# Performance work log

Hardware: AMD Instinct MI355X
Metric: run time of the kernel (lower is better)

Reference implementation:

```python
import jax, jax.numpy as jnp
import numpy as np

# ---- static configuration (from SSN.configure) ----
B, H, W = 2, 512, 512
N_SV = 1024
Kh = int(np.floor(np.sqrt(float(N_SV) * H / W)))  # 32
Kw = int(np.floor(np.sqrt(float(N_SV) * W / H)))  # 32
K = Kh * Kw                                       # 1024
P_SCALE = 0.4
LAB_SCALE = 0.26
SOFTSCALE = -1.0
NUM_STEPS = 5
YX_SCALE = max(Kh / (P_SCALE * H), Kw / (P_SCALE * W))
INVALID_DIST = 1e10


def setup_inputs() -> dict:
    key = jax.random.key(0)
    img_lab = jax.random.normal(key, (B, 3, H, W), dtype=jnp.float32)
    # regular-grid initial superpixel index, as SSN initializes it
    ys = (jnp.arange(H, dtype=jnp.int32) * Kh) // H   # (H,) in [0,Kh)
    xs = (jnp.arange(W, dtype=jnp.int32) * Kw) // W   # (W,) in [0,Kw)
    init = ys[:, None] * Kw + xs[None, :]             # (H,W) in [0,K)
    init_spIndx = jnp.broadcast_to(init, (B, H, W))
    return {"img_lab": img_lab, "init_spIndx": init_spIndx}


def _pfeat_yxlab(img_lab):
    # (B,5,H,W): scaled Y, X positions + scaled LAB color
    Y = jnp.broadcast_to(jnp.arange(H, dtype=img_lab.dtype)[None, None, :, None], (B, 1, H, W))
    X = jnp.broadcast_to(jnp.arange(W, dtype=img_lab.dtype)[None, None, None, :], (B, 1, H, W))
    return jnp.concatenate([YX_SCALE * Y, YX_SCALE * X, LAB_SCALE * img_lab], axis=1)


def _neighbor_indices(init_spIndx):
    # 3x3 superpixel-grid neighborhood of each pixel's init superpixel
    ki = init_spIndx // Kw  # (B,H,W)
    kj = init_spIndx % Kw
    offs = jnp.array([(di, dj) for di in (-1, 0, 1) for dj in (-1, 0, 1)], dtype=jnp.int32)  # (9,2)
    ni = ki[:, None] + offs[:, 0][None, :, None, None]  # (B,9,H,W)
    nj = kj[:, None] + offs[:, 1][None, :, None, None]
    valid = (ni >= 0) & (ni < Kh) & (nj >= 0) & (nj < Kw)
    idx = jnp.clip(ni, 0, Kh - 1) * Kw + jnp.clip(nj, 0, Kw - 1)  # (B,9,H,W) in [0,K)
    return idx, valid


def _seg_sum(vals, idx):
    # vals (B, C, N), idx (B, N) -> (B, C, K)
    return jax.vmap(lambda v, i: jax.ops.segment_sum(v.T, i, num_segments=K).T)(vals, idx)


def _sp_feat_gather(pFeat, init_spIndx):
    # spFeatGather2d: per-superpixel mean of pixel features -> (B,C,K)
    C = pFeat.shape[1]
    pf = pFeat.reshape(B, C, H * W)
    ix = init_spIndx.reshape(B, H * W)
    fsum = _seg_sum(pf, ix)
    cnt = jax.vmap(lambda i: jax.ops.segment_sum(jnp.ones((H * W,), jnp.float32), i, num_segments=K))(ix)
    return fsum / jnp.maximum(cnt, 1.0)[:, None, :]


def _psp_assoc(pFeat, spFeat, idx, valid):
    # softmax over 9 local superpixels of scaled squared distance
    nbr = jax.vmap(lambda sf, ix: sf[:, ix])(spFeat, idx)          # (B,C,9,H,W)
    dist = jnp.sum((pFeat[:, :, None] - nbr) ** 2, axis=1)          # (B,9,H,W)
    dist = jnp.where(valid, dist, INVALID_DIST)
    return jax.nn.softmax(SOFTSCALE * dist, axis=1)


def _sp_feat_update(pFeat, assoc, idx, valid):
    # spFeatUpdate2d: association-weighted scatter-mean into superpixels
    C = pFeat.shape[1]
    w = jnp.where(valid, assoc, 0.0)                                # (B,9,H,W)
    contrib = (pFeat[:, :, None] * w[:, None]).reshape(B, C, 9 * H * W)
    flat_i = idx.reshape(B, 9 * H * W)
    fsum = _seg_sum(contrib, flat_i)                                # (B,C,K)
    wsum = jax.vmap(lambda wv, i: jax.ops.segment_sum(wv, i, num_segments=K))(w.reshape(B, -1), flat_i)
    return fsum / jnp.maximum(wsum, 1e-10)[:, None, :]


def reference(img_lab, init_spIndx):
    pFeat = _pfeat_yxlab(img_lab)                      # (B,5,H,W)
    idx, valid = _neighbor_indices(init_spIndx)        # (B,9,H,W)
    spFeat = _sp_feat_gather(pFeat, init_spIndx)       # (B,5,K)
    for _ in range(1, NUM_STEPS):
        assoc = _psp_assoc(pFeat, spFeat, idx, valid)
        spFeat = _sp_feat_update(pFeat, assoc, idx, valid)
    psp_assoc = _psp_assoc(pFeat, spFeat, idx, valid)  # (B,9,H,W)
    rel = jnp.argmax(psp_assoc, axis=1)                # (B,H,W)
    final_spIndx = jnp.take_along_axis(idx, rel[:, None], axis=1)[:, 0]  # (B,H,W)
    return pFeat, spFeat, psp_assoc, final_spIndx
```

## Files before the change

### kernel.cpp

```cpp
#include <hip/hip_runtime.h>

namespace {
constexpr int B = 2, H = 512, W = 512;
constexpr int KH = 32, KW = 32, K = 1024;
constexpr int HW = H * W;
constexpr float YX_SCALE = 0.15625f;
constexpr float LAB_SCALE = 0.26f;
}

template <int CTRL>
__device__ __forceinline__ float dpp_add(float v) {
  int r = __builtin_amdgcn_update_dpp(0, __float_as_int(v), CTRL, 0xF, 0xF, true);
  return v + __int_as_float(r);
}
__device__ __forceinline__ float wave_sum64(float v) {
  v = dpp_add<0xB1>(v);
  v = dpp_add<0x4E>(v);
  v = dpp_add<0x141>(v);
  v = dpp_add<0x140>(v);
  v = dpp_add<0x142>(v);
  v = dpp_add<0x143>(v);
  return v;
}

__device__ __forceinline__ float fast_rcp(float x) { return __builtin_amdgcn_rcpf(x); }

__device__ __forceinline__ float gather54(const float* __restrict__ pin,
                                          int b, int ki, int kj, int lane) {
  float g = 0.0f;
  const int n = lane / 6, comp = lane % 6;
  const int nki = ki + n / 3 - 1, nkj = kj + n % 3 - 1;
  if ((unsigned)nki < (unsigned)KH && (unsigned)nkj < (unsigned)KW) {
#pragma unroll
    for (int j = 0; j < 9; ++j) {
      const int ci = nki - (j / 3 - 1), cj = nkj - (j % 3 - 1);
      if ((unsigned)ci < (unsigned)KH && (unsigned)cj < (unsigned)KW)
        g += pin[(size_t)((b << 10) + (ci << 5) + cj) * 54 + j * 6 + comp];
    }
  }
  return g;
}

__global__ __launch_bounds__(256) void ssn_init(const float* __restrict__ lab,
                                                float* __restrict__ outPFeat,
                                                float* __restrict__ partial) {
  const int cell = blockIdx.x;
  const int b = cell >> 10;
  const int k = cell & (K - 1);
  const int ki = k >> 5, kj = k & 31;
  const int t = threadIdx.x;
  const int y = (ki << 4) + (t >> 4);
  const int x = (kj << 4) + (t & 15);
  const int pix = y * W + x;
  const float* labB = lab + (size_t)b * 3 * HW;

  float f[5];
  f[0] = YX_SCALE * (float)y;
  f[1] = YX_SCALE * (float)x;
  f[2] = LAB_SCALE * labB[pix];
  f[3] = LAB_SCALE * labB[HW + pix];
  f[4] = LAB_SCALE * labB[2 * HW + pix];

  float* po = outPFeat + (size_t)b * 5 * HW + pix;
#pragma unroll
  for (int c = 0; c < 5; ++c) po[(size_t)c * HW] = f[c];

  if (t < 54 && (t < 24 || t >= 30)) partial[(size_t)cell * 54 + t] = 0.0f;

  float s[5];
#pragma unroll
  for (int c = 0; c < 5; ++c) s[c] = wave_sum64(f[c]);
  __shared__ float red[4][5];
  if ((t & 63) == 63) {
#pragma unroll
    for (int c = 0; c < 5; ++c) red[t >> 6][c] = s[c];
  }
  __syncthreads();
  if (t < 5)
    partial[(size_t)cell * 54 + 25 + t] = red[0][t] + red[1][t] + red[2][t] + red[3][t];
  if (t == 5) partial[(size_t)cell * 54 + 24] = 256.0f;
}

__global__ __launch_bounds__(256) void ssn_update2(const float* __restrict__ lab,
                                                   const float* __restrict__ pin,
                                                   float* __restrict__ pout) {
  __shared__ float sfg[2][54];
  __shared__ float comb[2][2][54];
  const int lane = threadIdx.x & 63;
  const int wid = threadIdx.x >> 6;
  const int cidx = wid >> 1, sub = wid & 1;
  const int cell = blockIdx.x * 2 + cidx;
  const int b = cell >> 10;
  const int k = cell & (K - 1);
  const int ki = k >> 5, kj = k & 31;

  if (wid < 2 && lane < 54) {
    const int gcell = blockIdx.x * 2 + wid;
    const int gk = gcell & (K - 1);
    sfg[wid][lane] = gather54(pin, gcell >> 10, gk >> 5, gk & 31, lane);
  }
  __syncthreads();

  float sf[9][5];
  bool valid[9];
#pragma unroll
  for (int n = 0; n < 9; ++n) {
    const int ni = ki + n / 3 - 1, nj = kj + n % 3 - 1;
    valid[n] = ((unsigned)ni < (unsigned)KH) && ((unsigned)nj < (unsigned)KW);
    const float inv = fast_rcp(fmaxf(sfg[cidx][n * 6], 1e-10f));
#pragma unroll
    for (int c = 0; c < 5; ++c) sf[n][c] = sfg[cidx][n * 6 + 1 + c] * inv;
  }

  float acc[54];
#pragma unroll
  for (int i = 0; i < 54; ++i) acc[i] = 0.0f;

  const float* labB = lab + (size_t)b * 3 * HW;
#pragma unroll
  for (int pxi = 0; pxi < 2; ++pxi) {
    const int t = lane + sub * 64 + pxi * 128;
    const int y = (ki << 4) + (t >> 4);
    const int x = (kj << 4) + (t & 15);
    const int pix = y * W + x;
    float f[5];
    f[0] = YX_SCALE * (float)y;
    f[1] = YX_SCALE * (float)x;
    f[2] = LAB_SCALE * labB[pix];
    f[3] = LAB_SCALE * labB[HW + pix];
    f[4] = LAB_SCALE * labB[2 * HW + pix];

    float d[9];
#pragma unroll
    for (int j = 0; j < 9; ++j) {
      float t0 = f[0] - sf[j][0];
      float dd = t0 * t0;
#pragma unroll
      for (int c = 1; c < 5; ++c) {
        const float tc = f[c] - sf[j][c];
        dd = fmaf(tc, tc, dd);
      }
      d[j] = dd;
    }
    float m = 1e30f;
#pragma unroll
    for (int j = 0; j < 9; ++j)
      if (valid[j]) m = fminf(m, d[j]);
    float e[9], sum = 0.0f;
#pragma unroll
    for (int j = 0; j < 9; ++j) {
      e[j] = valid[j] ? __expf(m - d[j]) : 0.0f;
      sum += e[j];
    }
    const float inv = fast_rcp(sum);
#pragma unroll
    for (int j = 0; j < 9; ++j) {
      const float w = e[j] * inv;
      acc[j * 6 + 0] += w;
#pragma unroll
      for (int c = 0; c < 5; ++c)
        acc[j * 6 + 1 + c] = fmaf(w, f[c], acc[j * 6 + 1 + c]);
    }
  }

#pragma unroll
  for (int i = 0; i < 54; ++i) acc[i] = wave_sum64(acc[i]);
  if (lane == 63) {
#pragma unroll
    for (int i = 0; i < 54; ++i) comb[sub][cidx][i] = acc[i];
  }
  __syncthreads();
  if (wid < 2 && lane < 54) {
    const int scell = blockIdx.x * 2 + wid;
    pout[(size_t)scell * 54 + lane] = comb[0][wid][lane] + comb[1][wid][lane];
  }
}

__global__ __launch_bounds__(256) void ssn_final2(const float* __restrict__ lab,
                                                  const float* __restrict__ pin,
                                                  float* __restrict__ outSpFeat,
                                                  float* __restrict__ outAssoc,
                                                  float* __restrict__ outIdx) {
  __shared__ float sfg[54];
  const int tid = threadIdx.x;
  const int cell = blockIdx.x;
  const int b = cell >> 10;
  const int k = cell & (K - 1);
  const int ki = k >> 5, kj = k & 31;

  if (tid < 54) sfg[tid] = gather54(pin, b, ki, kj, tid);
  __syncthreads();

  if (tid < 5) {
    const float inv4 = 1.0f / fmaxf(sfg[24], 1e-10f);
    outSpFeat[((size_t)b * 5 + tid) * K + k] = sfg[25 + tid] * inv4;
  }

  float sf[9][5];
  bool valid[9];
#pragma unroll
  for (int n = 0; n < 9; ++n) {
    const int ni = ki + n / 3 - 1, nj = kj + n % 3 - 1;
    valid[n] = ((unsigned)ni < (unsigned)KH) && ((unsigned)nj < (unsigned)KW);
    const float inv = 1.0f / fmaxf(sfg[n * 6], 1e-10f);
#pragma unroll
    for (int c = 0; c < 5; ++c) sf[n][c] = sfg[n * 6 + 1 + c] * inv;
  }

  const int y = (ki << 4) + (tid >> 4);
  const int x = (kj << 4) + (tid & 15);
  const int pix = y * W + x;
  const float* labB = lab + (size_t)b * 3 * HW;
  float f[5];
  f[0] = YX_SCALE * (float)y;
  f[1] = YX_SCALE * (float)x;
  f[2] = LAB_SCALE * labB[pix];
  f[3] = LAB_SCALE * labB[HW + pix];
  f[4] = LAB_SCALE * labB[2 * HW + pix];

  float d[9];
#pragma unroll
  for (int j = 0; j < 9; ++j) {
    float t0 = f[0] - sf[j][0];
    float dd = t0 * t0;
#pragma unroll
    for (int c = 1; c < 5; ++c) {
      const float tc = f[c] - sf[j][c];
      dd = fmaf(tc, tc, dd);
    }
    d[j] = dd;
  }
  float m = 1e30f;
#pragma unroll
  for (int j = 0; j < 9; ++j)
    if (valid[j]) m = fminf(m, d[j]);
  float e[9], sum = 0.0f;
#pragma unroll
  for (int j = 0; j < 9; ++j) {
    e[j] = valid[j] ? __expf(m - d[j]) : 0.0f;
    sum += e[j];
  }
  const float inv = 1.0f / sum;

  float* oa = outAssoc + (size_t)b * 9 * HW + pix;
#pragma unroll
  for (int j = 0; j < 9; ++j) oa[(size_t)j * HW] = e[j] * inv;

  int bestj = 4;
  float bestd = 1e30f;
#pragma unroll
  for (int j = 0; j < 9; ++j)
    if (valid[j] && d[j] < bestd) { bestd = d[j]; bestj = j; }
  const int bi = ki + bestj / 3 - 1;
  const int bj = kj + bestj % 3 - 1;
  outIdx[(size_t)b * HW + pix] = (float)(bi * KW + bj);
}

extern "C" void kernel_launch(void* const* d_in, const int* in_sizes, int n_in,
                              void* d_out, int out_size, void* d_ws, size_t ws_size,
                              hipStream_t stream) {
  const float* lab = (const float*)d_in[0];

  float* out = (float*)d_out;
  float* outPFeat = out;
  float* outSpFeat = outPFeat + 2621440;
  float* outAssoc = outSpFeat + 10240;
  float* outIdx = outAssoc + 4718592;

  float* pA = (float*)d_ws;
  float* pB = pA + (size_t)B * K * 54;

  ssn_init<<<B * K, 256, 0, stream>>>(lab, outPFeat, pA);
  ssn_update2<<<B * K / 2, 256, 0, stream>>>(lab, pA, pB);
  ssn_update2<<<B * K / 2, 256, 0, stream>>>(lab, pB, pA);
  ssn_update2<<<B * K / 2, 256, 0, stream>>>(lab, pA, pB);
  ssn_update2<<<B * K / 2, 256, 0, stream>>>(lab, pB, pA);
  ssn_final2<<<B * K, 256, 0, stream>>>(lab, pA, outSpFeat, outAssoc, outIdx);
}
```

Measured before the change: 117.7 us.

## Fuse init with first update step and restructure update to one cell per block

The init kernel now computes the initial superpixel means for the 3x3 neighbourhood directly by recomputing each neighbour cell's pixel sums, then runs the first association/update step in the same kernel. This removes one launch and one round trip of partial sums through global memory. The update kernel is changed to one cell per block with one pixel per thread, reducing over waves per neighbour instead of holding 54 register accumulators. The cost is nine times the lab reads in the fused init and more wave reductions per pixel.

Result: slower. 128.4 us (+9.0%).

```diff
diff --git a/kernel.cpp b/kernel.cpp
--- a/kernel.cpp
+++ b/kernel.cpp
@@ -6,6 +6,7 @@
 constexpr int HW = H * W;
 constexpr float YX_SCALE = 0.15625f;
 constexpr float LAB_SCALE = 0.26f;
+constexpr float INV256 = 1.0f / 256.0f;
 }
 
 template <int CTRL>
@@ -26,9 +27,9 @@
 __device__ __forceinline__ float fast_rcp(float x) { return __builtin_amdgcn_rcpf(x); }
 
 __device__ __forceinline__ float gather54(const float* __restrict__ pin,
-                                          int b, int ki, int kj, int lane) {
+                                          int b, int ki, int kj, int t) {
   float g = 0.0f;
-  const int n = lane / 6, comp = lane % 6;
+  const int n = t / 6, comp = t % 6;
   const int nki = ki + n / 3 - 1, nkj = kj + n % 3 - 1;
   if ((unsigned)nki < (unsigned)KH && (unsigned)nkj < (unsigned)KW) {
 #pragma unroll
@@ -41,19 +42,61 @@
   return g;
 }
 
-__global__ __launch_bounds__(256) void ssn_init(const float* __restrict__ lab,
-                                                float* __restrict__ outPFeat,
-                                                float* __restrict__ partial) {
+__global__ __launch_bounds__(256) void ssn_initu1(const float* __restrict__ lab,
+                                                  float* __restrict__ outPFeat,
+                                                  float* __restrict__ pout) {
+  __shared__ float nb[9][5];
+  __shared__ float comb[4][54];
+  const int t = threadIdx.x;
+  const int lane = t & 63;
+  const int wid = t >> 6;
   const int cell = blockIdx.x;
   const int b = cell >> 10;
   const int k = cell & (K - 1);
   const int ki = k >> 5, kj = k & 31;
-  const int t = threadIdx.x;
+  const float* labB = lab + (size_t)b * 3 * HW;
+
+#pragma unroll
+  for (int rep = 0; rep < 3; ++rep) {
+    const int n = wid + rep * 4;
+    if (n > 8) break;
+    const int ni = ki + n / 3 - 1, nj = kj + n % 3 - 1;
+    const bool v = ((unsigned)ni < (unsigned)KH) && ((unsigned)nj < (unsigned)KW);
+    float s0 = 0, s1 = 0, s2 = 0, s3 = 0, s4 = 0;
+    if (v) {
+#pragma unroll
+      for (int px = 0; px < 4; ++px) {
+        const int tt = lane + px * 64;
+        const int y = (ni << 4) + (tt >> 4);
+        const int x = (nj << 4) + (tt & 15);
+        const int pix = y * W + x;
+        const float a0 = LAB_SCALE * labB[pix];
+        const float a1 = LAB_SCALE * labB[HW + pix];
+        const float a2 = LAB_SCALE * labB[2 * HW + pix];
+        const float f0 = YX_SCALE * (float)y, f1 = YX_SCALE * (float)x;
+        if (n == 4) {
+          float* po = outPFeat + (size_t)b * 5 * HW + pix;
+          po[0] = f0;
+          po[HW] = f1;
+          po[2 * HW] = a0;
+          po[3 * HW] = a1;
+          po[4 * HW] = a2;
+        }
+        s0 += f0; s1 += f1; s2 += a0; s3 += a1; s4 += a2;
+      }
+      s0 = wave_sum64(s0); s1 = wave_sum64(s1); s2 = wave_sum64(s2);
+      s3 = wave_sum64(s3); s4 = wave_sum64(s4);
+    }
+    if (lane == 63) {
+      nb[n][0] = s0 * INV256; nb[n][1] = s1 * INV256; nb[n][2] = s2 * INV256;
+      nb[n][3] = s3 * INV256; nb[n][4] = s4 * INV256;
+    }
+  }
+  __syncthreads();
+
   const int y = (ki << 4) + (t >> 4);
   const int x = (kj << 4) + (t & 15);
   const int pix = y * W + x;
-  const float* labB = lab + (size_t)b * 3 * HW;
-
   float f[5];
   f[0] = YX_SCALE * (float)y;
   f[1] = YX_SCALE * (float)x;
@@ -61,44 +104,63 @@
   f[3] = LAB_SCALE * labB[HW + pix];
   f[4] = LAB_SCALE * labB[2 * HW + pix];
 
-  float* po = outPFeat + (size_t)b * 5 * HW + pix;
-#pragma unroll
-  for (int c = 0; c < 5; ++c) po[(size_t)c * HW] = f[c];
-
-  if (t < 54 && (t < 24 || t >= 30)) partial[(size_t)cell * 54 + t] = 0.0f;
-
-  float s[5];
-#pragma unroll
-  for (int c = 0; c < 5; ++c) s[c] = wave_sum64(f[c]);
-  __shared__ float red[4][5];
-  if ((t & 63) == 63) {
-#pragma unroll
-    for (int c = 0; c < 5; ++c) red[t >> 6][c] = s[c];
-  }
-  __syncthreads();
-  if (t < 5)
-    partial[(size_t)cell * 54 + 25 + t] = red[0][t] + red[1][t] + red[2][t] + red[3][t];
-  if (t == 5) partial[(size_t)cell * 54 + 24] = 256.0f;
-}
-
-__global__ __launch_bounds__(256) void ssn_update2(const float* __restrict__ lab,
+  float d[9];
+  bool valid[9];
+#pragma unroll
+  for (int j = 0; j < 9; ++j) {
+    const int ni = ki + j / 3 - 1, nj = kj + j % 3 - 1;
+    valid[j] = ((unsigned)ni < (unsigned)KH) && ((unsigned)nj < (unsigned)KW);
+    float t0 = f[0] - nb[j][0];
+    float dd = t0 * t0;
+#pragma unroll
+    for (int c = 1; c < 5; ++c) {
+      const float tc = f[c] - nb[j][c];
+      dd = fmaf(tc, tc, dd);
+    }
+    d[j] = dd;
+  }
+  float m = 1e30f;
+#pragma unroll
+  for (int j = 0; j < 9; ++j)
+    if (valid[j]) m = fminf(m, d[j]);
+  float e[9], sum = 0.0f;
+#pragma unroll
+  for (int j = 0; j < 9; ++j) {
+    e[j] = valid[j] ? __expf(m - d[j]) : 0.0f;
+    sum += e[j];
+  }
+  const float inv = fast_rcp(sum);
+
+#pragma unroll
+  for (int n9 = 0; n9 < 9; ++n9) {
+    const float w = e[n9] * inv;
+    float r = wave_sum64(w);
+    if (lane == 63) comb[wid][n9 * 6] = r;
+#pragma unroll
+    for (int c = 0; c < 5; ++c) {
+      r = wave_sum64(w * f[c]);
+      if (lane == 63) comb[wid][n9 * 6 + 1 + c] = r;
+    }
+  }
+  __syncthreads();
+  if (t < 54)
+    pout[(size_t)cell * 54 + t] = comb[0][t] + comb[1][t] + comb[2][t] + comb[3][t];
+}
+
+__global__ __launch_bounds__(256) void ssn_update3(const float* __restrict__ lab,
                                                    const float* __restrict__ pin,
                                                    float* __restrict__ pout) {
-  __shared__ float sfg[2][54];
-  __shared__ float comb[2][2][54];
-  const int lane = threadIdx.x & 63;
-  const int wid = threadIdx.x >> 6;
-  const int cidx = wid >> 1, sub = wid & 1;
-  const int cell = blockIdx.x * 2 + cidx;
+  __shared__ float sfg[54];
+  __shared__ float comb[4][54];
+  const int t = threadIdx.x;
+  const int lane = t & 63;
+  const int wid = t >> 6;
+  const int cell = blockIdx.x;
   const int b = cell >> 10;
   const int k = cell & (K - 1);
   const int ki = k >> 5, kj = k & 31;
 
-  if (wid < 2 && lane < 54) {
-    const int gcell = blockIdx.x * 2 + wid;
-    const int gk = gcell & (K - 1);
-    sfg[wid][lane] = gather54(pin, gcell >> 10, gk >> 5, gk & 31, lane);
-  }
+  if (t < 54) sfg[t] = gather54(pin, b, ki, kj, t);
   __syncthreads();
 
   float sf[9][5];
@@ -107,73 +169,60 @@
   for (int n = 0; n < 9; ++n) {
     const int ni = ki + n / 3 - 1, nj = kj + n % 3 - 1;
     valid[n] = ((unsigned)ni < (unsigned)KH) && ((unsigned)nj < (unsigned)KW);
-    const float inv = fast_rcp(fmaxf(sfg[cidx][n * 6], 1e-10f));
-#pragma unroll
-    for (int c = 0; c < 5; ++c) sf[n][c] = sfg[cidx][n * 6 + 1 + c] * inv;
-  }
-
-  float acc[54];
-#pragma unroll
-  for (int i = 0; i < 54; ++i) acc[i] = 0.0f;
-
+    const float inv = fast_rcp(fmaxf(sfg[n * 6], 1e-10f));
+#pragma unroll
+    for (int c = 0; c < 5; ++c) sf[n][c] = sfg[n * 6 + 1 + c] * inv;
+  }
+
+  const int y = (ki << 4) + (t >> 4);
+  const int x = (kj << 4) + (t & 15);
+  const int pix = y * W + x;
   const float* labB = lab + (size_t)b * 3 * HW;
-#pragma unroll
-  for (int pxi = 0; pxi < 2; ++pxi) {
-    const int t = lane + sub * 64 + pxi * 128;
-    const int y = (ki << 4) + (t >> 4);
-    const int x = (kj << 4) + (t & 15);
-    const int pix = y * W + x;
-    float f[5];
-    f[0] = YX_SCALE * (float)y;
-    f[1] = YX_SCALE * (float)x;
-    f[2] = LAB_SCALE * labB[pix];
-    f[3] = LAB_SCALE * labB[HW + pix];
-    f[4] = LAB_SCALE * labB[2 * HW + pix];
-
-    float d[9];
-#pragma unroll
-    for (int j = 0; j < 9; ++j) {
-      float t0 = f[0] - sf[j][0];
-      float dd = t0 * t0;
-#pragma unroll
-      for (int c = 1; c < 5; ++c) {
-        const float tc = f[c] - sf[j][c];
-        dd = fmaf(tc, tc, dd);
-      }
-      d[j] = dd;
-    }
-    float m = 1e30f;
-#pragma unroll
-    for (int j = 0; j < 9; ++j)
-      if (valid[j]) m = fminf(m, d[j]);
-    float e[9], sum = 0.0f;
-#pragma unroll
-    for (int j = 0; j < 9; ++j) {
-      e[j] = valid[j] ? __expf(m - d[j]) : 0.0f;
-      sum += e[j];
-    }
-    const float inv = fast_rcp(sum);
-#pragma unroll
-    for (int j = 0; j < 9; ++j) {
-      const float w = e[j] * inv;
-      acc[j * 6 + 0] += w;
-#pragma unroll
-      for (int c = 0; c < 5; ++c)
-        acc[j * 6 + 1 + c] = fmaf(w, f[c], acc[j * 6 + 1 + c]);
-    }
-  }
-
-#pragma unroll
-  for (int i = 0; i < 54; ++i) acc[i] = wave_sum64(acc[i]);
-  if (lane == 63) {
-#pragma unroll
-    for (int i = 0; i < 54; ++i) comb[sub][cidx][i] = acc[i];
-  }
-  __syncthreads();
-  if (wid < 2 && lane < 54) {
-    const int scell = blockIdx.x * 2 + wid;
-    pout[(size_t)scell * 54 + lane] = comb[0][wid][lane] + comb[1][wid][lane];
-  }
+  float f[5];
+  f[0] = YX_SCALE * (float)y;
+  f[1] = YX_SCALE * (float)x;
+  f[2] = LAB_SCALE * labB[pix];
+  f[3] = LAB_SCALE * labB[HW + pix];
+  f[4] = LAB_SCALE * labB[2 * HW + pix];
+
+  float d[9];
+#pragma unroll
+  for (int j = 0; j < 9; ++j) {
+    float t0 = f[0] - sf[j][0];
+    float dd = t0 * t0;
+#pragma unroll
+    for (int c = 1; c < 5; ++c) {
+      const float tc = f[c] - sf[j][c];
+      dd = fmaf(tc, tc, dd);
+    }
+    d[j] = dd;
+  }
+  float m = 1e30f;
+#pragma unroll
+  for (int j = 0; j < 9; ++j)
+    if (valid[j]) m = fminf(m, d[j]);
+  float e[9], sum = 0.0f;
+#pragma unroll
+  for (int j = 0; j < 9; ++j) {
+    e[j] = valid[j] ? __expf(m - d[j]) : 0.0f;
+    sum += e[j];
+  }
+  const float inv = fast_rcp(sum);
+
+#pragma unroll
+  for (int n9 = 0; n9 < 9; ++n9) {
+    const float w = e[n9] * inv;
+    float r = wave_sum64(w);
+    if (lane == 63) comb[wid][n9 * 6] = r;
+#pragma unroll
+    for (int c = 0; c < 5; ++c) {
+      r = wave_sum64(w * f[c]);
+      if (lane == 63) comb[wid][n9 * 6 + 1 + c] = r;
+    }
+  }
+  __syncthreads();
+  if (t < 54)
+    pout[(size_t)cell * 54 + t] = comb[0][t] + comb[1][t] + comb[2][t] + comb[3][t];
 }
 
 __global__ __launch_bounds__(256) void ssn_final2(const float* __restrict__ lab,
@@ -270,10 +319,9 @@
   float* pA = (float*)d_ws;
   float* pB = pA + (size_t)B * K * 54;
 
-  ssn_init<<<B * K, 256, 0, stream>>>(lab, outPFeat, pA);
-  ssn_update2<<<B * K / 2, 256, 0, stream>>>(lab, pA, pB);
-  ssn_update2<<<B * K / 2, 256, 0, stream>>>(lab, pB, pA);
-  ssn_update2<<<B * K / 2, 256, 0, stream>>>(lab, pA, pB);
-  ssn_update2<<<B * K / 2, 256, 0, stream>>>(lab, pB, pA);
-  ssn_final2<<<B * K, 256, 0, stream>>>(lab, pA, outSpFeat, outAssoc, outIdx);
-}
+  ssn_initu1<<<B * K, 256, 0, stream>>>(lab, outPFeat, pA);
+  ssn_update3<<<B * K, 256, 0, stream>>>(lab, pA, pB);
+  ssn_update3<<<B * K, 256, 0, stream>>>(lab, pB, pA);
+  ssn_update3<<<B * K, 256, 0, stream>>>(lab, pA, pB);
+  ssn_final2<<<B * K, 256, 0, stream>>>(lab, pB, outSpFeat, outAssoc, outIdx);
+}
```
